# Performance work log

Measured on AMD Instinct MI355X. Metric: run time of the kernel, lower is better.

The kernel has to match this reference:

```python
import jax, jax.numpy as jnp
import numpy as np

EPS = 1e-5
K = 20  # n. neighbors


def _lrelu(x):
    return jnp.where(x >= 0, x, 0.2 * x)


def _bn(x, gamma, beta):
    # training-mode batchnorm over all axes except channel axis 1
    axes = tuple(i for i in range(x.ndim) if i != 1)
    m = jnp.mean(x, axis=axes, keepdims=True)
    v = jnp.var(x, axis=axes, keepdims=True)
    shape = [1, x.shape[1]] + [1] * (x.ndim - 2)
    return (x - m) * jax.lax.rsqrt(v + EPS) * gamma.reshape(shape) + beta.reshape(shape)


def _knn(x, k):
    # x: (B, C, N) -> idx (B, N, k) of nearest neighbors (largest negative sq dist)
    xx = jnp.sum(x * x, axis=1)                      # (B, N)
    inner = jnp.einsum('bcn,bcm->bnm', x, x)          # (B, N, N)
    dist = -xx[:, :, None] + 2.0 * inner - xx[:, None, :]
    _, idx = jax.lax.top_k(dist, k)
    return idx


def _graph_feature(x, k):
    # x: (B, C, N) -> edge features (B, 2C, N, k)
    B = x.shape[0]
    idx = _knn(x, k)                                  # (B, N, k)
    xt = jnp.transpose(x, (0, 2, 1))                  # (B, N, C)
    nbr = xt[jnp.arange(B)[:, None, None], idx]       # (B, N, k, C)
    ctr = xt[:, :, None, :]                           # (B, N, 1, C)
    edge = jnp.concatenate([nbr - ctr, jnp.broadcast_to(ctr, nbr.shape)], axis=-1)
    return jnp.transpose(edge, (0, 3, 1, 2))          # (B, 2C, N, k)


def _conv1d(W, x):
    return jnp.einsum('oc,bcn->bon', W, x)


def _conv2d(W, x):
    return jnp.einsum('oc,bcnk->bonk', W, x)


def setup_inputs() -> dict:
    key = jax.random.key(0)
    ks = jax.random.split(key, 10)
    w = lambda k, s: jax.random.normal(k, s, jnp.float32) * 0.05
    d = {
        'x': jax.random.normal(ks[0], (4, 3, 4096), jnp.float32),
        'W1': w(ks[1], (64, 3)),
        'W2': w(ks[2], (64, 128)),
        'W3': w(ks[3], (64, 128)),
        'W4': w(ks[4], (512, 64)),
        'W5': w(ks[5], (512, 704)),
        'W6': w(ks[6], (256, 512)),
        'W7': w(ks[7], (128, 256)),
        'W8': w(ks[8], (2, 128)),
        'bias8': jnp.zeros((2,), jnp.float32),
    }
    bn_ch = [64, 64, 64, 512, 512, 256, 128]
    for i, c in enumerate(bn_ch, start=1):
        d[f'gamma{i}'] = jnp.ones((c,), jnp.float32)
        d[f'beta{i}'] = jnp.zeros((c,), jnp.float32)
    return d


def reference(x, W1, W2, W3, W4, W5, W6, W7, W8, bias8,
              gamma1, beta1, gamma2, beta2, gamma3, beta3, gamma4, beta4,
              gamma5, beta5, gamma6, beta6, gamma7, beta7):
    N = x.shape[2]
    x1 = _lrelu(_bn(_conv1d(W1, x), gamma1, beta1))                 # (B,64,N)
    e2 = _graph_feature(x1, K)                                      # (B,128,N,k)
    x2 = _lrelu(_bn(_conv2d(W2, e2), gamma2, beta2)).max(axis=-1)   # (B,64,N)
    e3 = _graph_feature(x2, K)
    x3 = _lrelu(_bn(_conv2d(W3, e3), gamma3, beta3)).max(axis=-1)   # (B,64,N)
    x6 = _lrelu(_bn(_conv1d(W4, x3), gamma4, beta4))                # (B,512,N)
    x6 = jnp.broadcast_to(x6.max(axis=-1, keepdims=True), (x6.shape[0], x6.shape[1], N))
    x7 = jnp.concatenate([x1, x2, x3, x6], axis=1)                  # (B,704,N)
    x7 = _lrelu(_bn(_conv1d(W5, x7), gamma5, beta5))
    x7 = _lrelu(_bn(_conv1d(W6, x7), gamma6, beta6))
    x7 = _lrelu(_bn(_conv1d(W7, x7), gamma7, beta7))
    return _conv1d(W8, x7) + bias8[None, :, None]                   # (B,2,N)
```

## Files before the change

kernel.cpp:

```cpp
#include <hip/hip_runtime.h>
#include <math.h>

#define NN 4096
#define BB 4
#define NPT (NN*BB)
#define KK 20
#define EPSB 1e-5f

#define AS_STRIDE 132
#define WS_STRIDE 68
#define SKEW(c) ((((((c)>>2)&7))<<2) + (((c)>>5)*28))

__device__ __forceinline__ float lrelu(float x){ return x >= 0.f ? x : 0.2f*x; }

__global__ void conv1_kernel(const float* __restrict__ x, const float* __restrict__ W1,
                             float* __restrict__ xcat){
  __shared__ float Wl[192];
  int tid = threadIdx.x;
  if (tid < 192) Wl[tid] = W1[tid];
  __syncthreads();
  int p = blockIdx.x*4 + (tid >> 6);
  int o = tid & 63;
  int b = p >> 12, n = p & 4095;
  const float* xb = x + (size_t)b*3*NN + n;
  float acc = Wl[o*3+0]*xb[0] + Wl[o*3+1]*xb[NN] + Wl[o*3+2]*xb[2*NN];
  xcat[(size_t)p*192 + o] = acc;
}

__global__ void stats_pm_kernel(const float* __restrict__ buf, int stride, int ofs,
                                float* __restrict__ psum, float* __restrict__ psumsq, int C){
  int tid = threadIdx.x;
  int lane = tid & 63, g = tid >> 6;
  int o = blockIdx.x*64 + lane;
  int p0 = blockIdx.y*256 + g*64;
  float s = 0.f, ss = 0.f;
  for (int i = 0; i < 64; ++i){
    float v = buf[(size_t)(p0+i)*stride + ofs + o];
    s += v; ss += v*v;
  }
  __shared__ float rs[4][64], rss[4][64];
  rs[g][lane] = s; rss[g][lane] = ss;
  __syncthreads();
  if (g == 0){
    s  = rs[0][lane]+rs[1][lane]+rs[2][lane]+rs[3][lane];
    ss = rss[0][lane]+rss[1][lane]+rss[2][lane]+rss[3][lane];
    psum[(size_t)blockIdx.y*C + o] = s;
    psumsq[(size_t)blockIdx.y*C + o] = ss;
  }
}

__global__ void bn_finalize_kernel(const float* __restrict__ psum, const float* __restrict__ psumsq,
                                   int nparts,
                                   const float* __restrict__ gamma, const float* __restrict__ beta,
                                   float* __restrict__ scale, float* __restrict__ shift,
                                   float invcnt, int C){
  int o = threadIdx.x + blockIdx.x*blockDim.x;
  if (o >= C) return;
  float s = 0.f, ss = 0.f;
  for (int i = 0; i < nparts; ++i){
    s  += psum[(size_t)i*C + o];
    ss += psumsq[(size_t)i*C + o];
  }
  float m = s*invcnt;
  float v = ss*invcnt - m*m;
  v = fmaxf(v, 0.f);
  float sc = gamma[o] * rsqrtf(v + EPSB);
  scale[o] = sc;
  shift[o] = beta[o] - m*sc;
}

__global__ void apply_bn_kernel(float* __restrict__ buf, int stride, int ofs, int log2C,
                                const float* __restrict__ scale, const float* __restrict__ shift){
  int i = blockIdx.x*256 + threadIdx.x;
  int o = i & ((1<<log2C)-1);
  int p = i >> log2C;
  size_t a = (size_t)p*stride + ofs + o;
  float e = buf[a]*scale[o] + shift[o];
  buf[a] = lrelu(e);
}

__global__ void xx_kernel(const float* __restrict__ xcat, int stride, int ofs,
                          float* __restrict__ xx){
  int p = blockIdx.x*256 + threadIdx.x;
  const float4* r = (const float4*)(xcat + (size_t)p*stride + ofs);
  float s = 0.f;
  #pragma unroll
  for (int i = 0; i < 16; ++i){ float4 v = r[i]; s += v.x*v.x + v.y*v.y + v.z*v.z + v.w*v.w; }
  xx[p] = s;
}

__global__ void __launch_bounds__(256, 2)
dist_kernel(const float* __restrict__ xcat, int ofs,
            const float* __restrict__ xx, float* __restrict__ dist, int b){
  int bx = blockIdx.x, by = blockIdx.y;
  if (by > bx) return;
  __shared__ float As[64*AS_STRIDE + 64];
  __shared__ float Bs[64*AS_STRIDE + 64];
  int tid = threadIdx.x;
  int n0 = by*128, m0 = bx*128;
  const float* base = xcat + (size_t)b*NN*192 + ofs;
  int cgrp = (tid & 15)*4;
  float4 vin[8], vw[8];
  #pragma unroll
  for (int j = 0; j < 8; ++j){
    int row = (tid + 256*j) >> 4;
    vin[j] = *(const float4*)(base + (size_t)(n0+row)*192 + cgrp);
    vw[j]  = *(const float4*)(base + (size_t)(m0+row)*192 + cgrp);
  }
  #pragma unroll
  for (int j = 0; j < 8; ++j){
    int row = (tid + 256*j) >> 4, c4 = cgrp;
    float4 v = vin[j];
    As[(c4+0)*AS_STRIDE+SKEW(c4+0)+row]=v.x; As[(c4+1)*AS_STRIDE+SKEW(c4+1)+row]=v.y;
    As[(c4+2)*AS_STRIDE+SKEW(c4+2)+row]=v.z; As[(c4+3)*AS_STRIDE+SKEW(c4+3)+row]=v.w;
    float4 w = vw[j];
    Bs[(c4+0)*AS_STRIDE+SKEW(c4+0)+row]=w.x; Bs[(c4+1)*AS_STRIDE+SKEW(c4+1)+row]=w.y;
    Bs[(c4+2)*AS_STRIDE+SKEW(c4+2)+row]=w.z; Bs[(c4+3)*AS_STRIDE+SKEW(c4+3)+row]=w.w;
  }
  __syncthreads();
  int pA = (tid >> 4)*4, oB = (tid & 15)*4;
  float acc[8][8] = {};
  for (int c = 0; c < 64; ++c){
    const float* arow = &As[c*AS_STRIDE + SKEW(c)];
    const float* brow = &Bs[c*AS_STRIDE + SKEW(c)];
    float4 a0 = *(const float4*)&arow[pA];
    float4 a1 = *(const float4*)&arow[pA + 64];
    float4 b0 = *(const float4*)&brow[oB];
    float4 b1 = *(const float4*)&brow[oB + 64];
    float av[8] = {a0.x,a0.y,a0.z,a0.w,a1.x,a1.y,a1.z,a1.w};
    float bv[8] = {b0.x,b0.y,b0.z,b0.w,b1.x,b1.y,b1.z,b1.w};
    #pragma unroll
    for (int i = 0; i < 8; ++i)
      #pragma unroll
      for (int j = 0; j < 8; ++j)
        acc[i][j] += av[i]*bv[j];
  }
  float xmv[8], xnv[8];
  #pragma unroll
  for (int j = 0; j < 4; ++j){
    xmv[j]   = xx[b*NN + m0 + oB + j];
    xmv[4+j] = xx[b*NN + m0 + 64 + oB + j];
    xnv[j]   = xx[b*NN + n0 + pA + j];
    xnv[4+j] = xx[b*NN + n0 + 64 + pA + j];
  }
  #pragma unroll
  for (int h = 0; h < 2; ++h){
    #pragma unroll
    for (int i = 0; i < 4; ++i){
      int row = n0 + h*64 + pA + i;
      float xn = xnv[h*4 + i];
      int ai = h*4 + i;
      float4 w0, w1;
      w0.x = 2.f*acc[ai][0] - xn - xmv[0]; w0.y = 2.f*acc[ai][1] - xn - xmv[1];
      w0.z = 2.f*acc[ai][2] - xn - xmv[2]; w0.w = 2.f*acc[ai][3] - xn - xmv[3];
      w1.x = 2.f*acc[ai][4] - xn - xmv[4]; w1.y = 2.f*acc[ai][5] - xn - xmv[5];
      w1.z = 2.f*acc[ai][6] - xn - xmv[6]; w1.w = 2.f*acc[ai][7] - xn - xmv[7];
      float* drow = dist + (size_t)row*NN + m0;
      *(float4*)(drow + oB) = w0;
      *(float4*)(drow + 64 + oB) = w1;
    }
  }
  if (bx != by){
    #pragma unroll
    for (int jh = 0; jh < 2; ++jh){
      #pragma unroll
      for (int jj = 0; jj < 4; ++jj){
        int j = jh*4 + jj;
        float xm = xmv[j];
        float4 lo, hi;
        lo.x = 2.f*acc[0][j] - xm - xnv[0];
        lo.y = 2.f*acc[1][j] - xm - xnv[1];
        lo.z = 2.f*acc[2][j] - xm - xnv[2];
        lo.w = 2.f*acc[3][j] - xm - xnv[3];
        hi.x = 2.f*acc[4][j] - xm - xnv[4];
        hi.y = 2.f*acc[5][j] - xm - xnv[5];
        hi.z = 2.f*acc[6][j] - xm - xnv[6];
        hi.w = 2.f*acc[7][j] - xm - xnv[7];
        float* drow = dist + (size_t)(m0 + jh*64 + oB + jj)*NN + n0;
        *(float4*)(drow + pA) = lo;
        *(float4*)(drow + 64 + pA) = hi;
      }
    }
  }
}

__global__ void topk_kernel(const float* __restrict__ dist, int* __restrict__ idxout){
  int n = blockIdx.x;
  int tid = threadIdx.x;
  int wv = tid >> 6;
  const float* row = dist + (size_t)n*NN;
  unsigned k[16];
  #pragma unroll
  for (int i = 0; i < 16; ++i){
    unsigned u = __float_as_uint(row[tid + (i<<8)]);
    k[i] = u ^ (unsigned)(((int)u >> 31) | 0x80000000);
  }
  __shared__ unsigned hist[4][256];
  __shared__ unsigned sufx[257];
  __shared__ unsigned selw[1];
  __shared__ unsigned toff[256];
  __shared__ int mred[4];
  unsigned remaining = KK;
  unsigned prefix = 0;
  #pragma unroll
  for (int lvl = 0; lvl < 4; ++lvl){
    int shift = 24 - lvl*8;
    hist[0][tid]=0; hist[1][tid]=0; hist[2][tid]=0; hist[3][tid]=0;
    __syncthreads();
    unsigned pmask = (lvl == 0) ? 0u : (0xFFFFFFFFu << (shift + 8));
    #pragma unroll
    for (int i = 0; i < 16; ++i){
      if ((k[i] & pmask) == prefix)
        atomicAdd(&hist[wv][(k[i] >> shift) & 255], 1u);
    }
    __syncthreads();
    if (tid < 64){
      unsigned h[4];
      #pragma unroll
      for (int q = 0; q < 4; ++q)
        h[q] = hist[0][tid*4+q]+hist[1][tid*4+q]+hist[2][tid*4+q]+hist[3][tid*4+q];
      unsigned lane_sum = h[0]+h[1]+h[2]+h[3];
      unsigned acc = lane_sum;
      #pragma unroll
      for (int s = 1; s < 64; s <<= 1){
        unsigned o = __shfl_down(acc, s);
        if (tid + s < 64) acc += o;
      }
      unsigned excl = acc - lane_sum;
      sufx[tid*4+3] = excl + h[3];
      sufx[tid*4+2] = excl + h[3] + h[2];
      sufx[tid*4+1] = excl + h[3] + h[2] + h[1];
      sufx[tid*4+0] = excl + h[3] + h[2] + h[1] + h[0];
      if (tid == 0) sufx[256] = 0;
    }
    __syncthreads();
    unsigned s_d = sufx[tid], s_d1 = sufx[tid+1];
    if (s_d >= remaining && s_d1 < remaining) selw[0] = tid;
    __syncthreads();
    unsigned d = selw[0];
    remaining -= sufx[d+1];
    prefix |= d << shift;
  }
  unsigned K20 = prefix;
  unsigned r = remaining;
  unsigned mycount = 0;
  #pragma unroll
  for (int i = 0; i < 16; ++i) if (k[i] > K20) mycount++;
  toff[tid] = mycount;
  __syncthreads();
  if (tid < 64){
    unsigned c0=toff[tid*4], c1=toff[tid*4+1], c2=toff[tid*4+2], c3=toff[tid*4+3];
    unsigned lane_sum = c0+c1+c2+c3;
    unsigned acc = lane_sum;
    #pragma unroll
    for (int s = 1; s < 64; s <<= 1){
      unsigned o = __shfl_up(acc, s);
      if ((int)tid - s >= 0) acc += o;
    }
    unsigned excl = acc - lane_sum;
    sufx[tid*4+0] = excl;
    sufx[tid*4+1] = excl + c0;
    sufx[tid*4+2] = excl + c0 + c1;
    sufx[tid*4+3] = excl + c0 + c1 + c2;
  }
  __syncthreads();
  unsigned pos = sufx[tid];
  int* orow = idxout + n*KK;
  #pragma unroll
  for (int i = 0; i < 16; ++i)
    if (k[i] > K20) orow[pos++] = tid + (i<<8);
  unsigned A = KK - r;
  int last = -1;
  for (unsigned t = 0; t < r; ++t){
    int best = 0x7fffffff;
    #pragma unroll
    for (int i = 0; i < 16; ++i){
      int m = tid + (i<<8);
      if (k[i] == K20 && m > last && m < best) best = m;
    }
    #pragma unroll
    for (int s = 32; s > 0; s >>= 1){
      int o = __shfl_down(best, s);
      best = min(best, o);
    }
    if ((tid & 63) == 0) mred[tid >> 6] = best;
    __syncthreads();
    int w = min(min(mred[0],mred[1]), min(mred[2],mred[3]));
    if (tid == 0) orow[A + t] = w;
    last = w;
    __syncthreads();
  }
}

__global__ void ut_kernel(const float* __restrict__ xcat, int ofs, const float* __restrict__ W,
                          float* __restrict__ U, float* __restrict__ T){
  __shared__ float Wl[64*129];
  int tid = threadIdx.x;
  for (int i = tid; i < 64*128; i += 256){
    int o = i >> 7, c = i & 127;
    Wl[o*129 + c] = W[i];
  }
  __syncthreads();
  int g = tid >> 6, lane = tid & 63;
  int p = blockIdx.x*4 + g;
  float xv = xcat[(size_t)p*192 + ofs + lane];
  const float* wr = Wl + lane*129;
  float u = 0.f, t = 0.f;
  for (int c = 0; c < 64; ++c){
    float xc = __shfl(xv, c);
    float wa = wr[c], wb = wr[64+c];
    u += wa*xc;
    t += (wb - wa)*xc;
  }
  U[(size_t)p*64 + lane] = u;
  T[(size_t)p*64 + lane] = t;
}

__global__ void gather_kernel(const float* __restrict__ U, const float* __restrict__ T,
                              const int* __restrict__ idx,
                              float* __restrict__ psum, float* __restrict__ psumsq,
                              float* __restrict__ vmax, float* __restrict__ vmin){
  int tid = threadIdx.x;
  int g = tid >> 6, lane = tid & 63;
  int p0 = blockIdx.x*64 + g*16;
  float s = 0.f, ss = 0.f;
  for (int pi = 0; pi < 16; ++pi){
    int p = p0 + pi;
    int base = (p >> 12) << 12;
    float t = T[(size_t)p*64 + lane];
    const int* ir = idx + (size_t)p*KK;
    float mx = -INFINITY, mn = INFINITY;
    for (int k = 0; k < KK; ++k){
      int j = ir[k];
      float v = U[(size_t)(base + j)*64 + lane] + t;
      s += v; ss += v*v;
      mx = fmaxf(mx, v); mn = fminf(mn, v);
    }
    vmax[(size_t)p*64 + lane] = mx;
    vmin[(size_t)p*64 + lane] = mn;
  }
  __shared__ float rs[4][64], rss[4][64];
  rs[g][lane] = s; rss[g][lane] = ss;
  __syncthreads();
  if (g == 0){
    s  = rs[0][lane]+rs[1][lane]+rs[2][lane]+rs[3][lane];
    ss = rss[0][lane]+rss[1][lane]+rss[2][lane]+rss[3][lane];
    psum[(size_t)blockIdx.x*64 + lane] = s;
    psumsq[(size_t)blockIdx.x*64 + lane] = ss;
  }
}

__global__ void gapply_kernel(const float* __restrict__ vmax, const float* __restrict__ vmin,
                              const float* __restrict__ scale, const float* __restrict__ shift,
                              float* __restrict__ xcat, int ofs){
  int i = blockIdx.x*256 + threadIdx.x;
  int p = i >> 6, o = i & 63;
  float s = scale[o];
  float v = (s >= 0.f) ? vmax[i] : vmin[i];
  xcat[(size_t)p*192 + ofs + o] = lrelu(s*v + shift[o]);
}

__global__ void __launch_bounds__(256, 2)
mm_kernel(const float* __restrict__ in, int inStride, int inOfs,
          const float* __restrict__ W, int wStride,
          float* __restrict__ out, int outStride,
          const float* __restrict__ bias, int O, int I,
          const float* __restrict__ bnScale, const float* __restrict__ bnShift){
  __shared__ float As[64*AS_STRIDE + 64];
  __shared__ float Ws[64*WS_STRIDE + 64];
  int tid = threadIdx.x;
  int p0 = blockIdx.x*128, o0 = blockIdx.y*64;
  int psub = (tid >> 4)*8, osub = (tid & 15)*4;
  int cgrp = (tid & 15)*4;
  float acc[8][4] = {};
  for (int cc = 0; cc < I; cc += 64){
    float4 sc4 = make_float4(1.f,1.f,1.f,1.f), sh4 = make_float4(0.f,0.f,0.f,0.f);
    if (bnScale){
      sc4 = *(const float4*)(bnScale + cc + cgrp);
      sh4 = *(const float4*)(bnShift + cc + cgrp);
    }
    float4 vin[8], vw[4];
    #pragma unroll
    for (int j = 0; j < 8; ++j){
      int row = (tid + 256*j) >> 4;
      vin[j] = *(const float4*)(in + (size_t)(p0+row)*inStride + inOfs + cc + cgrp);
    }
    #pragma unroll
    for (int j = 0; j < 4; ++j){
      int row = (tid + 256*j) >> 4;
      vw[j] = *(const float4*)(W + (size_t)(o0+row)*wStride + cc + cgrp);
    }
    #pragma unroll
    for (int j = 0; j < 8; ++j){
      int row = (tid + 256*j) >> 4, c4 = cgrp;
      float4 v = vin[j];
      if (bnScale){
        v.x = lrelu(v.x*sc4.x + sh4.x); v.y = lrelu(v.y*sc4.y + sh4.y);
        v.z = lrelu(v.z*sc4.z + sh4.z); v.w = lrelu(v.w*sc4.w + sh4.w);
      }
      As[(c4+0)*AS_STRIDE+SKEW(c4+0)+row]=v.x; As[(c4+1)*AS_STRIDE+SKEW(c4+1)+row]=v.y;
      As[(c4+2)*AS_STRIDE+SKEW(c4+2)+row]=v.z; As[(c4+3)*AS_STRIDE+SKEW(c4+3)+row]=v.w;
    }
    #pragma unroll
    for (int j = 0; j < 4; ++j){
      int row = (tid + 256*j) >> 4, c4 = cgrp;
      float4 v = vw[j];
      Ws[(c4+0)*WS_STRIDE+SKEW(c4+0)+row]=v.x; Ws[(c4+1)*WS_STRIDE+SKEW(c4+1)+row]=v.y;
      Ws[(c4+2)*WS_STRIDE+SKEW(c4+2)+row]=v.z; Ws[(c4+3)*WS_STRIDE+SKEW(c4+3)+row]=v.w;
    }
    __syncthreads();
    for (int c = 0; c < 64; ++c){
      const float* arow = &As[c*AS_STRIDE + SKEW(c)];
      const float* brow = &Ws[c*WS_STRIDE + SKEW(c)];
      float4 a0 = *(const float4*)&arow[psub];
      float4 a1 = *(const float4*)&arow[psub + 4];
      float4 bb = *(const float4*)&brow[osub];
      float av[8] = {a0.x,a0.y,a0.z,a0.w,a1.x,a1.y,a1.z,a1.w};
      float bv[4] = {bb.x,bb.y,bb.z,bb.w};
      #pragma unroll
      for (int i = 0; i < 8; ++i)
        #pragma unroll
        for (int j = 0; j < 4; ++j)
          acc[i][j] += av[i]*bv[j];
    }
    __syncthreads();
  }
  int bIdx = p0 >> 12;
  float bb0=0.f, bb1=0.f, bb2=0.f, bb3=0.f;
  if (bias){
    bb0 = bias[bIdx*O + o0 + osub + 0];
    bb1 = bias[bIdx*O + o0 + osub + 1];
    bb2 = bias[bIdx*O + o0 + osub + 2];
    bb3 = bias[bIdx*O + o0 + osub + 3];
  }
  #pragma unroll
  for (int i = 0; i < 8; ++i){
    float4 w;
    w.x = acc[i][0]+bb0; w.y = acc[i][1]+bb1; w.z = acc[i][2]+bb2; w.w = acc[i][3]+bb3;
    *(float4*)(out + (size_t)(p0+psub+i)*outStride + o0 + osub) = w;
  }
}

__global__ void __launch_bounds__(256, 2)
mm128_kernel(const float* __restrict__ in, int inStride, int inOfs,
             const float* __restrict__ W, int wStride,
             float* __restrict__ out, int outStride,
             const float* __restrict__ bias, int O, int I,
             const float* __restrict__ bnScale, const float* __restrict__ bnShift){
  __shared__ float As[64*AS_STRIDE + 64];
  __shared__ float Ws[64*AS_STRIDE + 64];
  int tid = threadIdx.x;
  int p0 = blockIdx.x*128, o0 = blockIdx.y*128;
  int pA = (tid >> 4)*4, oB = (tid & 15)*4;
  int cgrp = (tid & 15)*4;
  float acc[8][8] = {};
  for (int cc = 0; cc < I; cc += 64){
    float4 sc4 = make_float4(1.f,1.f,1.f,1.f), sh4 = make_float4(0.f,0.f,0.f,0.f);
    if (bnScale){
      sc4 = *(const float4*)(bnScale + cc + cgrp);
      sh4 = *(const float4*)(bnShift + cc + cgrp);
    }
    float4 vin[8], vw[8];
    #pragma unroll
    for (int j = 0; j < 8; ++j){
      int row = (tid + 256*j) >> 4;
      vin[j] = *(const float4*)(in + (size_t)(p0+row)*inStride + inOfs + cc + cgrp);
      vw[j]  = *(const float4*)(W + (size_t)(o0+row)*wStride + cc + cgrp);
    }
    #pragma unroll
    for (int j = 0; j < 8; ++j){
      int row = (tid + 256*j) >> 4, c4 = cgrp;
      float4 v = vin[j];
      if (bnScale){
        v.x = lrelu(v.x*sc4.x + sh4.x); v.y = lrelu(v.y*sc4.y + sh4.y);
        v.z = lrelu(v.z*sc4.z + sh4.z); v.w = lrelu(v.w*sc4.w + sh4.w);
      }
      As[(c4+0)*AS_STRIDE+SKEW(c4+0)+row]=v.x; As[(c4+1)*AS_STRIDE+SKEW(c4+1)+row]=v.y;
      As[(c4+2)*AS_STRIDE+SKEW(c4+2)+row]=v.z; As[(c4+3)*AS_STRIDE+SKEW(c4+3)+row]=v.w;
      float4 w = vw[j];
      Ws[(c4+0)*AS_STRIDE+SKEW(c4+0)+row]=w.x; Ws[(c4+1)*AS_STRIDE+SKEW(c4+1)+row]=w.y;
      Ws[(c4+2)*AS_STRIDE+SKEW(c4+2)+row]=w.z; Ws[(c4+3)*AS_STRIDE+SKEW(c4+3)+row]=w.w;
    }
    __syncthreads();
    for (int c = 0; c < 64; ++c){
      const float* arow = &As[c*AS_STRIDE + SKEW(c)];
      const float* brow = &Ws[c*AS_STRIDE + SKEW(c)];
      float4 a0 = *(const float4*)&arow[pA];
      float4 a1 = *(const float4*)&arow[pA + 64];
      float4 b0 = *(const float4*)&brow[oB];
      float4 b1 = *(const float4*)&brow[oB + 64];
      float av[8] = {a0.x,a0.y,a0.z,a0.w,a1.x,a1.y,a1.z,a1.w};
      float bv[8] = {b0.x,b0.y,b0.z,b0.w,b1.x,b1.y,b1.z,b1.w};
      #pragma unroll
      for (int i = 0; i < 8; ++i)
        #pragma unroll
        for (int j = 0; j < 8; ++j)
          acc[i][j] += av[i]*bv[j];
    }
    __syncthreads();
  }
  int bIdx = p0 >> 12;
  float bb[8] = {0.f,0.f,0.f,0.f,0.f,0.f,0.f,0.f};
  if (bias){
    #pragma unroll
    for (int j = 0; j < 4; ++j){
      bb[j]   = bias[bIdx*O + o0 + oB + j];
      bb[4+j] = bias[bIdx*O + o0 + 64 + oB + j];
    }
  }
  #pragma unroll
  for (int h = 0; h < 2; ++h){
    #pragma unroll
    for (int i = 0; i < 4; ++i){
      int row = p0 + h*64 + pA + i;
      int ai = h*4 + i;
      float4 w0, w1;
      w0.x = acc[ai][0]+bb[0]; w0.y = acc[ai][1]+bb[1];
      w0.z = acc[ai][2]+bb[2]; w0.w = acc[ai][3]+bb[3];
      w1.x = acc[ai][4]+bb[4]; w1.y = acc[ai][5]+bb[5];
      w1.z = acc[ai][6]+bb[6]; w1.w = acc[ai][7]+bb[7];
      float* orow = out + (size_t)row*outStride + o0;
      *(float4*)(orow + oB) = w0;
      *(float4*)(orow + 64 + oB) = w1;
    }
  }
}

__global__ void __launch_bounds__(256, 2)
conv4stats_kernel(const float* __restrict__ xcat, const float* __restrict__ W4,
                  float* __restrict__ psum, float* __restrict__ psumsq,
                  float* __restrict__ pmax, float* __restrict__ pmin){
  __shared__ float As[64*AS_STRIDE + 64];
  __shared__ float Ws[64*AS_STRIDE + 64];
  int tid = threadIdx.x;
  int p0 = blockIdx.x*128, o0 = blockIdx.y*128;
  int pA = (tid >> 4)*4, oB = (tid & 15)*4;
  int cgrp = (tid & 15)*4;
  float4 vin[8], vw[8];
  #pragma unroll
  for (int j = 0; j < 8; ++j){
    int row = (tid + 256*j) >> 4;
    vin[j] = *(const float4*)(xcat + (size_t)(p0+row)*192 + 128 + cgrp);
    vw[j]  = *(const float4*)(W4 + (size_t)(o0+row)*64 + cgrp);
  }
  #pragma unroll
  for (int j = 0; j < 8; ++j){
    int row = (tid + 256*j) >> 4, c4 = cgrp;
    float4 v = vin[j];
    As[(c4+0)*AS_STRIDE+SKEW(c4+0)+row]=v.x; As[(c4+1)*AS_STRIDE+SKEW(c4+1)+row]=v.y;
    As[(c4+2)*AS_STRIDE+SKEW(c4+2)+row]=v.z; As[(c4+3)*AS_STRIDE+SKEW(c4+3)+row]=v.w;
    float4 w = vw[j];
    Ws[(c4+0)*AS_STRIDE+SKEW(c4+0)+row]=w.x; Ws[(c4+1)*AS_STRIDE+SKEW(c4+1)+row]=w.y;
    Ws[(c4+2)*AS_STRIDE+SKEW(c4+2)+row]=w.z; Ws[(c4+3)*AS_STRIDE+SKEW(c4+3)+row]=w.w;
  }
  __syncthreads();
  float acc[8][8] = {};
  for (int c = 0; c < 64; ++c){
    const float* arow = &As[c*AS_STRIDE + SKEW(c)];
    const float* brow = &Ws[c*AS_STRIDE + SKEW(c)];
    float4 a0 = *(const float4*)&arow[pA];
    float4 a1 = *(const float4*)&arow[pA + 64];
    float4 b0 = *(const float4*)&brow[oB];
    float4 b1 = *(const float4*)&brow[oB + 64];
    float av[8] = {a0.x,a0.y,a0.z,a0.w,a1.x,a1.y,a1.z,a1.w};
    float bv[8] = {b0.x,b0.y,b0.z,b0.w,b1.x,b1.y,b1.z,b1.w};
    #pragma unroll
    for (int i = 0; i < 8; ++i)
      #pragma unroll
      for (int j = 0; j < 8; ++j)
        acc[i][j] += av[i]*bv[j];
  }
  float cs[8], cq[8], cmx[8], cmn[8];
  #pragma unroll
  for (int j = 0; j < 8; ++j){
    float s = 0.f, q = 0.f, mx = -INFINITY, mn = INFINITY;
    #pragma unroll
    for (int i = 0; i < 8; ++i){
      float v = acc[i][j];
      s += v; q += v*v; mx = fmaxf(mx, v); mn = fminf(mn, v);
    }
    cs[j]=s; cq[j]=q; cmx[j]=mx; cmn[j]=mn;
  }
  __syncthreads();
  int r = tid >> 4;
  #pragma unroll
  for (int j = 0; j < 8; ++j){
    int col = (j < 4) ? (oB + j) : (64 + oB + (j-4));
    As[r*128 + col]        = cs[j];
    As[2048 + r*128 + col] = cq[j];
    Ws[r*128 + col]        = cmx[j];
    Ws[2048 + r*128 + col] = cmn[j];
  }
  __syncthreads();
  if (tid < 128){
    float ts = 0.f, tq = 0.f, tm = -INFINITY, tn = INFINITY;
    for (int rr = 0; rr < 16; ++rr){
      ts += As[rr*128 + tid];
      tq += As[2048 + rr*128 + tid];
      tm = fmaxf(tm, Ws[rr*128 + tid]);
      tn = fminf(tn, Ws[2048 + rr*128 + tid]);
    }
    size_t slot = (size_t)blockIdx.x*512 + o0 + tid;
    psum[slot] = ts; psumsq[slot] = tq; pmax[slot] = tm; pmin[slot] = tn;
  }
}

__global__ void x6v_kernel(const float* __restrict__ pmax, const float* __restrict__ pmin,
                           const float* __restrict__ scale, const float* __restrict__ shift,
                           float* __restrict__ x6v){
  int t = blockIdx.x*256 + threadIdx.x;
  int b = t >> 9, o = t & 511;
  float mx = -INFINITY, mn = INFINITY;
  for (int pt = b*32; pt < b*32+32; ++pt){
    mx = fmaxf(mx, pmax[(size_t)pt*512 + o]);
    mn = fminf(mn, pmin[(size_t)pt*512 + o]);
  }
  float s = scale[o];
  float v = (s >= 0.f) ? mx : mn;
  x6v[t] = lrelu(s*v + shift[o]);
}

__global__ void bias5_kernel(const float* __restrict__ W5, const float* __restrict__ x6v,
                             float* __restrict__ b5){
  __shared__ float xl[512];
  int tid = threadIdx.x;
  int t = blockIdx.x*256 + tid;
  int b = t >> 9, o = t & 511;
  for (int i = tid; i < 512; i += 256) xl[i] = x6v[(b<<9) + i];
  __syncthreads();
  const float* wr = W5 + (size_t)o*704 + 192;
  float acc = 0.f;
  for (int c = 0; c < 512; ++c) acc += wr[c]*xl[c];
  b5[t] = acc;
}

__global__ void conv8_kernel(const float* __restrict__ r7, const float* __restrict__ W8,
                             const float* __restrict__ bias8,
                             const float* __restrict__ scale, const float* __restrict__ shift,
                             float* __restrict__ out){
  __shared__ float Wl[256];
  __shared__ float scl[128], shl[128];
  int tid = threadIdx.x;
  Wl[tid] = W8[tid];
  if (tid < 128){ scl[tid] = scale[tid]; shl[tid] = shift[tid]; }
  __syncthreads();
  int p = blockIdx.x*256 + tid;
  int b = p >> 12, n = p & 4095;
  const float4* row = (const float4*)(r7 + (size_t)p*128);
  float a0 = 0.f, a1 = 0.f;
  #pragma unroll
  for (int i = 0; i < 32; ++i){
    float4 v = row[i];
    v.x = lrelu(v.x*scl[i*4+0] + shl[i*4+0]);
    v.y = lrelu(v.y*scl[i*4+1] + shl[i*4+1]);
    v.z = lrelu(v.z*scl[i*4+2] + shl[i*4+2]);
    v.w = lrelu(v.w*scl[i*4+3] + shl[i*4+3]);
    a0 += v.x*Wl[i*4] + v.y*Wl[i*4+1] + v.z*Wl[i*4+2] + v.w*Wl[i*4+3];
    a1 += v.x*Wl[128+i*4] + v.y*Wl[128+i*4+1] + v.z*Wl[128+i*4+2] + v.w*Wl[128+i*4+3];
  }
  out[(size_t)(b*2+0)*NN + n] = a0 + bias8[0];
  out[(size_t)(b*2+1)*NN + n] = a1 + bias8[1];
}

extern "C" void kernel_launch(void* const* d_in, const int* in_sizes, int n_in,
                              void* d_out, int out_size, void* d_ws, size_t ws_size,
                              hipStream_t stream){
  const float* x     = (const float*)d_in[0];
  const float* W1    = (const float*)d_in[1];
  const float* W2    = (const float*)d_in[2];
  const float* W3    = (const float*)d_in[3];
  const float* W4    = (const float*)d_in[4];
  const float* W5    = (const float*)d_in[5];
  const float* W6    = (const float*)d_in[6];
  const float* W7    = (const float*)d_in[7];
  const float* W8    = (const float*)d_in[8];
  const float* bias8 = (const float*)d_in[9];
  const float* gamma[8]; const float* beta[8];
  for (int i = 1; i <= 7; ++i){
    gamma[i] = (const float*)d_in[10 + 2*(i-1)];
    beta[i]  = (const float*)d_in[11 + 2*(i-1)];
  }
  float* out = (float*)d_out;

  float* ws = (float*)d_ws;
  size_t off = 0;
  float* xcat  = ws + off; off += (size_t)NPT*192;
  float* U     = ws + off; off += (size_t)NPT*64;
  float* T     = ws + off; off += (size_t)NPT*64;
  float* xx    = ws + off; off += NPT;
  int*   idx   = (int*)(ws + off); off += (size_t)NPT*KK;
  float* psum  = ws + off; off += 128*512;
  float* psumsq= ws + off; off += 128*512;
  float* pmax  = ws + off; off += 128*512;
  float* pmin  = ws + off; off += 128*512;
  float* scale = ws + off; off += 512;
  float* shift = ws + off; off += 512;
  float* x6v   = ws + off; off += 2048;
  float* b5    = ws + off; off += 2048;
  float* big   = ws + off;
  float* dist  = big;
  float* vmaxB = big;
  float* vminB = big + (size_t)NPT*64;
  float* r5    = big;
  float* r6    = big + (size_t)NPT*512;
  float* r7    = big + (size_t)NPT*512 + (size_t)NPT*256;

  conv1_kernel<<<NPT/4, 256, 0, stream>>>(x, W1, xcat);
  stats_pm_kernel<<<dim3(1,64), 256, 0, stream>>>(xcat, 192, 0, psum, psumsq, 64);
  bn_finalize_kernel<<<1, 64, 0, stream>>>(psum, psumsq, 64, gamma[1], beta[1], scale, shift, 1.f/16384.f, 64);
  apply_bn_kernel<<<NPT*64/256, 256, 0, stream>>>(xcat, 192, 0, 6, scale, shift);

  xx_kernel<<<NPT/256, 256, 0, stream>>>(xcat, 192, 0, xx);
  for (int b = 0; b < BB; ++b){
    dist_kernel<<<dim3(32,32), 256, 0, stream>>>(xcat, 0, xx, dist, b);
    topk_kernel<<<NN, 256, 0, stream>>>(dist, idx + (size_t)b*NN*KK);
  }

  ut_kernel<<<NPT/4, 256, 0, stream>>>(xcat, 0, W2, U, T);
  gather_kernel<<<256, 256, 0, stream>>>(U, T, idx, psum, psumsq, vmaxB, vminB);
  bn_finalize_kernel<<<1, 64, 0, stream>>>(psum, psumsq, 256, gamma[2], beta[2], scale, shift, 1.f/327680.f, 64);
  gapply_kernel<<<NPT*64/256, 256, 0, stream>>>(vmaxB, vminB, scale, shift, xcat, 64);

  xx_kernel<<<NPT/256, 256, 0, stream>>>(xcat, 192, 64, xx);
  for (int b = 0; b < BB; ++b){
    dist_kernel<<<dim3(32,32), 256, 0, stream>>>(xcat, 64, xx, dist, b);
    topk_kernel<<<NN, 256, 0, stream>>>(dist, idx + (size_t)b*NN*KK);
  }

  ut_kernel<<<NPT/4, 256, 0, stream>>>(xcat, 64, W3, U, T);
  gather_kernel<<<256, 256, 0, stream>>>(U, T, idx, psum, psumsq, vmaxB, vminB);
  bn_finalize_kernel<<<1, 64, 0, stream>>>(psum, psumsq, 256, gamma[3], beta[3], scale, shift, 1.f/327680.f, 64);
  gapply_kernel<<<NPT*64/256, 256, 0, stream>>>(vmaxB, vminB, scale, shift, xcat, 128);

  conv4stats_kernel<<<dim3(NPT/128, 4), 256, 0, stream>>>(xcat, W4, psum, psumsq, pmax, pmin);
  bn_finalize_kernel<<<1, 512, 0, stream>>>(psum, psumsq, 128, gamma[4], beta[4], scale, shift, 1.f/16384.f, 512);
  x6v_kernel<<<8, 256, 0, stream>>>(pmax, pmin, scale, shift, x6v);
  bias5_kernel<<<8, 256, 0, stream>>>(W5, x6v, b5);

  mm128_kernel<<<dim3(NPT/128, 4), 256, 0, stream>>>(xcat, 192, 0, W5, 704, r5, 512, b5, 512, 192, nullptr, nullptr);
  stats_pm_kernel<<<dim3(8,64), 256, 0, stream>>>(r5, 512, 0, psum, psumsq, 512);
  bn_finalize_kernel<<<1, 512, 0, stream>>>(psum, psumsq, 64, gamma[5], beta[5], scale, shift, 1.f/16384.f, 512);

  mm128_kernel<<<dim3(NPT/128, 2), 256, 0, stream>>>(r5, 512, 0, W6, 512, r6, 256, nullptr, 256, 512, scale, shift);
  stats_pm_kernel<<<dim3(4,64), 256, 0, stream>>>(r6, 256, 0, psum, psumsq, 256);
  bn_finalize_kernel<<<1, 256, 0, stream>>>(psum, psumsq, 64, gamma[6], beta[6], scale, shift, 1.f/16384.f, 256);

  mm_kernel<<<dim3(NPT/128, 2), 256, 0, stream>>>(r6, 256, 0, W7, 256, r7, 128, nullptr, 128, 256, scale, shift);
  stats_pm_kernel<<<dim3(2,64), 256, 0, stream>>>(r7, 128, 0, psum, psumsq, 128);
  bn_finalize_kernel<<<1, 128, 0, stream>>>(psum, psumsq, 64, gamma[7], beta[7], scale, shift, 1.f/16384.f, 128);

  conv8_kernel<<<NPT/256, 256, 0, stream>>>(r7, W8, bias8, scale, shift, out);
}
```

Before: 1.348 ms.

## Replace block radix-select top-k with per-wave register insertion sort and merge

The top-k kernel changes from one 256-thread block per row doing a 4-level radix histogram select with many block barriers to one wavefront per row. Each lane keeps a sorted 20-entry list in registers over its 64 strided elements, then 20 rounds of wave shuffle-argmax merge the lists. This removes the shared-memory atomics and __syncthreads, at the cost of heavy register use for the 40-entry arrays and serial insertion work per lane.

```diff
diff --git a/kernel.cpp b/kernel.cpp
--- a/kernel.cpp
+++ b/kernel.cpp
@@ -185,110 +185,47 @@
 }
 
 __global__ void topk_kernel(const float* __restrict__ dist, int* __restrict__ idxout){
-  int n = blockIdx.x;
-  int tid = threadIdx.x;
-  int wv = tid >> 6;
+  int wv = threadIdx.x >> 6, lane = threadIdx.x & 63;
+  int n = blockIdx.x*4 + wv;
   const float* row = dist + (size_t)n*NN;
-  unsigned k[16];
-  #pragma unroll
-  for (int i = 0; i < 16; ++i){
-    unsigned u = __float_as_uint(row[tid + (i<<8)]);
-    k[i] = u ^ (unsigned)(((int)u >> 31) | 0x80000000);
-  }
-  __shared__ unsigned hist[4][256];
-  __shared__ unsigned sufx[257];
-  __shared__ unsigned selw[1];
-  __shared__ unsigned toff[256];
-  __shared__ int mred[4];
-  unsigned remaining = KK;
-  unsigned prefix = 0;
-  #pragma unroll
-  for (int lvl = 0; lvl < 4; ++lvl){
-    int shift = 24 - lvl*8;
-    hist[0][tid]=0; hist[1][tid]=0; hist[2][tid]=0; hist[3][tid]=0;
-    __syncthreads();
-    unsigned pmask = (lvl == 0) ? 0u : (0xFFFFFFFFu << (shift + 8));
-    #pragma unroll
-    for (int i = 0; i < 16; ++i){
-      if ((k[i] & pmask) == prefix)
-        atomicAdd(&hist[wv][(k[i] >> shift) & 255], 1u);
-    }
-    __syncthreads();
-    if (tid < 64){
-      unsigned h[4];
+  unsigned rv[KK], ri[KK];
+  #pragma unroll
+  for (int q = 0; q < KK; ++q){ rv[q] = 0u; ri[q] = 0xFFFFFFFFu; }
+  for (int i = 0; i < 64; ++i){
+    unsigned u = __float_as_uint(row[i*64 + lane]);
+    u ^= (unsigned)(((int)u >> 31) | 0x80000000);
+    unsigned ix = (unsigned)(i*64 + lane);
+    bool beat = (u > rv[KK-1]) || (u == rv[KK-1] && ix < ri[KK-1]);
+    if (beat){
+      unsigned pv = u, pi = ix;
       #pragma unroll
-      for (int q = 0; q < 4; ++q)
-        h[q] = hist[0][tid*4+q]+hist[1][tid*4+q]+hist[2][tid*4+q]+hist[3][tid*4+q];
-      unsigned lane_sum = h[0]+h[1]+h[2]+h[3];
-      unsigned acc = lane_sum;
+      for (int p = 0; p < KK; ++p){
+        bool keep = (rv[p] > pv) || (rv[p] == pv && ri[p] < pi);
+        unsigned nv = keep ? rv[p] : pv;
+        unsigned ni = keep ? ri[p] : pi;
+        pv = keep ? pv : rv[p];
+        pi = keep ? pi : ri[p];
+        rv[p] = nv; ri[p] = ni;
+      }
+    }
+  }
+  int* orow = idxout + (size_t)n*KK;
+  for (int q = 0; q < KK; ++q){
+    unsigned bv = rv[0], bi = ri[0];
+    #pragma unroll
+    for (int s = 1; s < 64; s <<= 1){
+      unsigned ov = __shfl_xor(bv, s);
+      unsigned oi = __shfl_xor(bi, s);
+      bool take = (ov > bv) || (ov == bv && oi < bi);
+      bv = take ? ov : bv;
+      bi = take ? oi : bi;
+    }
+    if (rv[0] == bv && ri[0] == bi){
       #pragma unroll
-      for (int s = 1; s < 64; s <<= 1){
-        unsigned o = __shfl_down(acc, s);
-        if (tid + s < 64) acc += o;
-      }
-      unsigned excl = acc - lane_sum;
-      sufx[tid*4+3] = excl + h[3];
-      sufx[tid*4+2] = excl + h[3] + h[2];
-      sufx[tid*4+1] = excl + h[3] + h[2] + h[1];
-      sufx[tid*4+0] = excl + h[3] + h[2] + h[1] + h[0];
-      if (tid == 0) sufx[256] = 0;
-    }
-    __syncthreads();
-    unsigned s_d = sufx[tid], s_d1 = sufx[tid+1];
-    if (s_d >= remaining && s_d1 < remaining) selw[0] = tid;
-    __syncthreads();
-    unsigned d = selw[0];
-    remaining -= sufx[d+1];
-    prefix |= d << shift;
-  }
-  unsigned K20 = prefix;
-  unsigned r = remaining;
-  unsigned mycount = 0;
-  #pragma unroll
-  for (int i = 0; i < 16; ++i) if (k[i] > K20) mycount++;
-  toff[tid] = mycount;
-  __syncthreads();
-  if (tid < 64){
-    unsigned c0=toff[tid*4], c1=toff[tid*4+1], c2=toff[tid*4+2], c3=toff[tid*4+3];
-    unsigned lane_sum = c0+c1+c2+c3;
-    unsigned acc = lane_sum;
-    #pragma unroll
-    for (int s = 1; s < 64; s <<= 1){
-      unsigned o = __shfl_up(acc, s);
-      if ((int)tid - s >= 0) acc += o;
-    }
-    unsigned excl = acc - lane_sum;
-    sufx[tid*4+0] = excl;
-    sufx[tid*4+1] = excl + c0;
-    sufx[tid*4+2] = excl + c0 + c1;
-    sufx[tid*4+3] = excl + c0 + c1 + c2;
-  }
-  __syncthreads();
-  unsigned pos = sufx[tid];
-  int* orow = idxout + n*KK;
-  #pragma unroll
-  for (int i = 0; i < 16; ++i)
-    if (k[i] > K20) orow[pos++] = tid + (i<<8);
-  unsigned A = KK - r;
-  int last = -1;
-  for (unsigned t = 0; t < r; ++t){
-    int best = 0x7fffffff;
-    #pragma unroll
-    for (int i = 0; i < 16; ++i){
-      int m = tid + (i<<8);
-      if (k[i] == K20 && m > last && m < best) best = m;
-    }
-    #pragma unroll
-    for (int s = 32; s > 0; s >>= 1){
-      int o = __shfl_down(best, s);
-      best = min(best, o);
-    }
-    if ((tid & 63) == 0) mred[tid >> 6] = best;
-    __syncthreads();
-    int w = min(min(mred[0],mred[1]), min(mred[2],mred[3]));
-    if (tid == 0) orow[A + t] = w;
-    last = w;
-    __syncthreads();
+      for (int p = 0; p < KK-1; ++p){ rv[p] = rv[p+1]; ri[p] = ri[p+1]; }
+      rv[KK-1] = 0u; ri[KK-1] = 0xFFFFFFFFu;
+    }
+    if (lane == 0) orow[q] = (int)bi;
   }
 }
 
@@ -713,7 +650,7 @@
   xx_kernel<<<NPT/256, 256, 0, stream>>>(xcat, 192, 0, xx);
   for (int b = 0; b < BB; ++b){
     dist_kernel<<<dim3(32,32), 256, 0, stream>>>(xcat, 0, xx, dist, b);
-    topk_kernel<<<NN, 256, 0, stream>>>(dist, idx + (size_t)b*NN*KK);
+    topk_kernel<<<NN/4, 256, 0, stream>>>(dist, idx + (size_t)b*NN*KK);
   }
 
   ut_kernel<<<NPT/4, 256, 0, stream>>>(xcat, 0, W2, U, T);
@@ -724,7 +661,7 @@
   xx_kernel<<<NPT/256, 256, 0, stream>>>(xcat, 192, 64, xx);
   for (int b = 0; b < BB; ++b){
     dist_kernel<<<dim3(32,32), 256, 0, stream>>>(xcat, 64, xx, dist, b);
-    topk_kernel<<<NN, 256, 0, stream>>>(dist, idx + (size_t)b*NN*KK);
+    topk_kernel<<<NN/4, 256, 0, stream>>>(dist, idx + (size_t)b*NN*KK);
   }
 
   ut_kernel<<<NPT/4, 256, 0, stream>>>(xcat, 64, W3, U, T);
```

Measured after the change: 1.748 ms. +29.7%, slower.
